# Performance work log

Hardware: AMD Instinct MI355X
Metric: run time of the kernel (lower is better)

The kernel has to match this reference:

```python
import jax, jax.numpy as jnp
import numpy as np

N_NODES = 100000
N_GRAPHS = 64
NEG_SLOPE = 0.1


def lrelu(x):
    return jnp.where(x > 0, x, NEG_SLOPE * x)


def gcn_layer(x, W, b, src, dst, deg_inv_sqrt):
    # PyG GCNConv: x' = D^-1/2 (A + I) D^-1/2 (x W) + b
    h = x @ W  # [N, out]
    norm = (deg_inv_sqrt[src] * deg_inv_sqrt[dst])[:, None]  # [E, 1]
    agg = jax.ops.segment_sum(h[src] * norm, dst, num_segments=N_NODES)
    agg = agg + h * (deg_inv_sqrt ** 2)[:, None]  # self-loop contribution
    return agg + b


def setup_inputs() -> dict:
    key = jax.random.key(0)
    ks = jax.random.split(key, 12)
    E = 1600000
    x = jax.random.normal(ks[0], (N_NODES, 128), dtype=jnp.float32)
    edge_index = jax.random.randint(ks[1], (2, E), 0, N_NODES, dtype=jnp.int32)
    batch = jnp.sort(jax.random.randint(ks[2], (N_NODES,), 0, N_GRAPHS, dtype=jnp.int32))

    def glorot(k, shape):
        fan_in, fan_out = shape
        s = jnp.sqrt(6.0 / (fan_in + fan_out))
        return jax.random.uniform(k, shape, jnp.float32, -s, s)

    return {
        "x": x,
        "edge_index": edge_index,
        "batch": batch,
        "W1": glorot(ks[3], (128, 32)),
        "b1": jnp.zeros((32,), jnp.float32),
        "W2": glorot(ks[4], (32, 64)),
        "b2": jnp.zeros((64,), jnp.float32),
        "Wl1": glorot(ks[5], (64, 128)),
        "bl1": jnp.zeros((128,), jnp.float32),
        "Wl2": glorot(ks[6], (128, 64)),
        "bl2": jnp.zeros((64,), jnp.float32),
        "Wl3": glorot(ks[7], (64, 1)),
        "bl3": jnp.zeros((1,), jnp.float32),
    }


def reference(x, edge_index, batch, W1, b1, W2, b2, Wl1, bl1, Wl2, bl2, Wl3, bl3):
    src, dst = edge_index[0], edge_index[1]
    # degree with self-loops (symmetric norm, all edge weights = 1)
    deg = jax.ops.segment_sum(jnp.ones_like(src, dtype=x.dtype), dst, num_segments=N_NODES) + 1.0
    deg_inv_sqrt = jax.lax.rsqrt(deg)

    h = lrelu(gcn_layer(x, W1, b1, src, dst, deg_inv_sqrt))
    h = gcn_layer(h, W2, b2, src, dst, deg_inv_sqrt)
    g = jax.ops.segment_max(h, batch, num_segments=N_GRAPHS)  # global max pool [G, 64]
    g = lrelu(g @ Wl1 + bl1)
    g = lrelu(g @ Wl2 + bl2)
    return g @ Wl3 + bl3  # [G, 1]
```

## Files before the change

### kernel.cpp

```cpp
#include <hip/hip_runtime.h>
#include <hip/hip_fp16.h>
#include <math.h>

#define N_NODES 100000
#define N_EDGES 1600000
#define N_GRAPHS 64
#define NB 391
#define CAP 5504

__device__ __forceinline__ unsigned f2o(float f) {
    unsigned u = __float_as_uint(f);
    return (u & 0x80000000u) ? ~u : (u | 0x80000000u);
}
__device__ __forceinline__ float o2f(unsigned u) {
    return (u & 0x80000000u) ? __uint_as_float(u & 0x7fffffffu) : __uint_as_float(~u);
}

__device__ __forceinline__ float4 cvt8(float2 raw) {
    __half2 h0 = ((const __half2*)&raw)[0];
    __half2 h1 = ((const __half2*)&raw)[1];
    float2 f0 = __half22float2(h0);
    float2 f1 = __half22float2(h1);
    return make_float4(f0.x, f0.y, f1.x, f1.y);
}
__device__ __forceinline__ float4 loadh8(const __half* p) {
    return cvt8(*(const float2*)p);
}
__device__ __forceinline__ void storeh8(__half* p, float4 v) {
    __half2 o0 = __floats2half2_rn(v.x, v.y);
    __half2 o1 = __floats2half2_rn(v.z, v.w);
    float2 ow;
    ((__half2*)&ow)[0] = o0;
    ((__half2*)&ow)[1] = o1;
    *(float2*)p = ow;
}

typedef _Float16 h2r __attribute__((ext_vector_type(2)));
typedef _Float16 h4  __attribute__((ext_vector_type(4)));
union HB { float4 f4; h2r h[4]; };
union H4 { float2 f2; h4 h; };

__global__ __launch_bounds__(256) void bucket_kernel(const int* __restrict__ src, const int* __restrict__ dst,
                                                     int* __restrict__ bucketCursor, unsigned* __restrict__ ebuf) {
    __shared__ int hist[NB];
    __shared__ int cur[NB];
    int tid = threadIdx.x;
    for (int b = tid; b < NB; b += 256) hist[b] = 0;
    __syncthreads();
    int e0 = blockIdx.x * 3200;
    for (int i = tid; i < 3200; i += 256) {
        int d = dst[e0 + i];
        atomicAdd(&hist[d >> 8], 1);
    }
    __syncthreads();
    for (int b = tid; b < NB; b += 256) {
        int h = hist[b];
        cur[b] = h ? atomicAdd(&bucketCursor[b], h) : 0;
    }
    __syncthreads();
    for (int i = tid; i < 3200; i += 256) {
        int d = dst[e0 + i];
        int s = src[e0 + i];
        int bu = d >> 8;
        int pos = atomicAdd(&cur[bu], 1);
        if (pos < CAP)
            ebuf[(size_t)bu * CAP + pos] = ((unsigned)(d & 255) << 24) | (unsigned)s;
    }
}

__global__ __launch_bounds__(256) void csr_kernel(const unsigned* __restrict__ ebuf,
                                                  const int* __restrict__ bucketCursor,
                                                  int* __restrict__ colb, int* __restrict__ rowptr,
                                                  int* __restrict__ cnt, float* __restrict__ dis) {
    __shared__ unsigned stage[CAP];
    __shared__ int c256[256], row256[256], cur256[256];
    int b = blockIdx.x;
    int tid = threadIdx.x;
    int M = bucketCursor[b];
    if (M > CAP) M = CAP;
    c256[tid] = 0;
    __syncthreads();
    const unsigned* eb = ebuf + (size_t)b * CAP;
    for (int i = tid; i < M; i += 256) atomicAdd(&c256[eb[i] >> 24], 1);
    __syncthreads();
    if (tid < 64) {
        int c0 = c256[tid * 4], c1 = c256[tid * 4 + 1], c2 = c256[tid * 4 + 2], c3 = c256[tid * 4 + 3];
        int s = c0 + c1 + c2 + c3;
        int inc = s;
        #pragma unroll
        for (int o = 1; o < 64; o <<= 1) {
            int v = __shfl_up(inc, o, 64);
            if (tid >= o) inc += v;
        }
        int ex = inc - s;
        row256[tid * 4] = ex;
        row256[tid * 4 + 1] = ex + c0;
        row256[tid * 4 + 2] = ex + c0 + c1;
        row256[tid * 4 + 3] = ex + c0 + c1 + c2;
    }
    __syncthreads();
    cur256[tid] = row256[tid];
    int node = (b << 8) + tid;
    if (node < N_NODES) {
        int c = c256[tid];
        cnt[node] = c;
        dis[node] = rsqrtf((float)(c + 1));
        rowptr[node] = b * CAP + row256[tid];
    }
    __syncthreads();
    for (int i = tid; i < M; i += 256) {
        unsigned p = eb[i];
        int slot = atomicAdd(&cur256[p >> 24], 1);
        stage[slot] = p & 0xFFFFFFu;
    }
    __syncthreads();
    for (int i = tid; i < M; i += 256) colb[b * CAP + i] = (int)stage[i];
}

__global__ __launch_bounds__(256) void gemm1_kernel(const float* __restrict__ x, const float* __restrict__ W1,
                                                    const float* __restrict__ dis, __half* __restrict__ hs1h) {
    __shared__ __half xsh[128][136];
    __shared__ __half wth[32][136];
    int tid = threadIdx.x;
    int r0 = blockIdx.x * 128;
    for (int idx = tid; idx < 128 * 32; idx += 256) {
        int k = idx >> 5, j = idx & 31;
        wth[j][k] = __float2half_rn(W1[idx]);
    }
    for (int idx = tid; idx < 128 * 32; idx += 256) {
        int r = idx >> 5, c4 = idx & 31;
        int gr = r0 + r;
        float4 v = (gr < N_NODES) ? ((const float4*)x)[(size_t)gr * 32 + c4] : make_float4(0.f, 0.f, 0.f, 0.f);
        __half* p = &xsh[r][c4 * 4];
        *(__half2*)p       = __floats2half2_rn(v.x, v.y);
        *(__half2*)(p + 2) = __floats2half2_rn(v.z, v.w);
    }
    __syncthreads();
    int jg = tid & 7;
    int rg = tid >> 3;
    float acc[4][4];
    #pragma unroll
    for (int i = 0; i < 4; i++)
        #pragma unroll
        for (int j = 0; j < 4; j++) acc[i][j] = 0.f;
    for (int kc = 0; kc < 128; kc += 8) {
        HB xr[4], wr[4];
        #pragma unroll
        for (int ri = 0; ri < 4; ri++) xr[ri].f4 = *(const float4*)&xsh[rg + 32 * ri][kc];
        #pragma unroll
        for (int jj = 0; jj < 4; jj++) wr[jj].f4 = *(const float4*)&wth[jg * 4 + jj][kc];
        #pragma unroll
        for (int ri = 0; ri < 4; ri++) {
            #pragma unroll
            for (int jj = 0; jj < 4; jj++) {
                #pragma unroll
                for (int t = 0; t < 4; t++) {
#if defined(__has_builtin) && __has_builtin(__builtin_amdgcn_fdot2)
                    acc[ri][jj] = __builtin_amdgcn_fdot2(xr[ri].h[t], wr[jj].h[t], acc[ri][jj], false);
#else
                    acc[ri][jj] += (float)xr[ri].h[t][0] * (float)wr[jj].h[t][0]
                                 + (float)xr[ri].h[t][1] * (float)wr[jj].h[t][1];
#endif
                }
            }
        }
    }
    #pragma unroll
    for (int ri = 0; ri < 4; ri++) {
        int gr = r0 + rg + 32 * ri;
        if (gr < N_NODES) {
            float dr = dis[gr];
            float2 ow;
            ((__half2*)&ow)[0] = __floats2half2_rn(dr * acc[ri][0], dr * acc[ri][1]);
            ((__half2*)&ow)[1] = __floats2half2_rn(dr * acc[ri][2], dr * acc[ri][3]);
            *(float2*)&hs1h[(size_t)gr * 32 + jg * 4] = ow;
        }
    }
}

__global__ __launch_bounds__(256) void agg1_kernel(const __half* __restrict__ hs1h, const int* __restrict__ colb,
                                                   const int* __restrict__ rowptr, const int* __restrict__ cnt,
                                                   const float* __restrict__ dis, const float* __restrict__ b1,
                                                   __half* __restrict__ t1h) {
    int tid = threadIdx.x;
    int wid = tid >> 6;
    int lane = tid & 63;
    int half = lane >> 5;
    int es = (lane >> 3) & 3;
    int q = lane & 7;
    int w = blockIdx.x * 4 + wid;
    int r0 = w * 4;

    H4 z; z.f2 = make_float2(0.f, 0.f);
    int r = r0 + half;
    int st = rowptr[r];
    int n = cnt[r];
    H4 pS = z, p0 = z, p1 = z, p2 = z, p3 = z, p4 = z, p5 = z;
    if (es == 0) pS.f2 = *(const float2*)(hs1h + (size_t)r * 32 + q * 4);
    {
        int e0 = es, e1 = 4 + es, e2 = 8 + es, e3 = 12 + es, e4 = 16 + es, e5 = 20 + es;
        if (e0 < n) p0.f2 = *(const float2*)(hs1h + (size_t)colb[st + e0] * 32 + q * 4);
        if (e1 < n) p1.f2 = *(const float2*)(hs1h + (size_t)colb[st + e1] * 32 + q * 4);
        if (e2 < n) p2.f2 = *(const float2*)(hs1h + (size_t)colb[st + e2] * 32 + q * 4);
        if (e3 < n) p3.f2 = *(const float2*)(hs1h + (size_t)colb[st + e3] * 32 + q * 4);
        if (e4 < n) p4.f2 = *(const float2*)(hs1h + (size_t)colb[st + e4] * 32 + q * 4);
        if (e5 < n) p5.f2 = *(const float2*)(hs1h + (size_t)colb[st + e5] * 32 + q * 4);
    }
    #pragma unroll
    for (int i = 0; i < 2; i++) {
        int rA = r;
        int stA = st, nA = n;
        H4 rS = pS, v0 = p0, v1 = p1, v2 = p2, v3 = p3, v4 = p4, v5 = p5;
        pS = z; p0 = z; p1 = z; p2 = z; p3 = z; p4 = z; p5 = z;
        if (i == 0) {
            r = r0 + 2 + half;
            st = rowptr[r];
            n = cnt[r];
            if (es == 0) pS.f2 = *(const float2*)(hs1h + (size_t)r * 32 + q * 4);
            int e0 = es, e1 = 4 + es, e2 = 8 + es, e3 = 12 + es, e4 = 16 + es, e5 = 20 + es;
            if (e0 < n) p0.f2 = *(const float2*)(hs1h + (size_t)colb[st + e0] * 32 + q * 4);
            if (e1 < n) p1.f2 = *(const float2*)(hs1h + (size_t)colb[st + e1] * 32 + q * 4);
            if (e2 < n) p2.f2 = *(const float2*)(hs1h + (size_t)colb[st + e2] * 32 + q * 4);
            if (e3 < n) p3.f2 = *(const float2*)(hs1h + (size_t)colb[st + e3] * 32 + q * 4);
            if (e4 < n) p4.f2 = *(const float2*)(hs1h + (size_t)colb[st + e4] * 32 + q * 4);
            if (e5 < n) p5.f2 = *(const float2*)(hs1h + (size_t)colb[st + e5] * 32 + q * 4);
        }
        h4 sh = (rS.h + (v0.h + v1.h)) + ((v2.h + v3.h) + (v4.h + v5.h));
        float4 a = make_float4((float)sh.x, (float)sh.y, (float)sh.z, (float)sh.w);
        for (int k = 24; k < nA; k += 8) {
            int e0 = k + es, e1 = k + 4 + es;
            if (e0 < nA) {
                float4 v = loadh8(hs1h + (size_t)colb[stA + e0] * 32 + q * 4);
                a.x += v.x; a.y += v.y; a.z += v.z; a.w += v.w;
            }
            if (e1 < nA) {
                float4 v = loadh8(hs1h + (size_t)colb[stA + e1] * 32 + q * 4);
                a.x += v.x; a.y += v.y; a.z += v.z; a.w += v.w;
            }
        }
        #pragma unroll
        for (int m = 8; m <= 16; m <<= 1) {
            a.x += __shfl_xor(a.x, m, 64);
            a.y += __shfl_xor(a.y, m, 64);
            a.z += __shfl_xor(a.z, m, 64);
            a.w += __shfl_xor(a.w, m, 64);
        }
        if (es == 0) {
            float4 bv = *(const float4*)&b1[q * 4];
            float dr = dis[rA];
            float4 v;
            v.x = dr * a.x + bv.x; v.y = dr * a.y + bv.y; v.z = dr * a.z + bv.z; v.w = dr * a.w + bv.w;
            v.x = v.x > 0.f ? v.x : 0.1f * v.x;
            v.y = v.y > 0.f ? v.y : 0.1f * v.y;
            v.z = v.z > 0.f ? v.z : 0.1f * v.z;
            v.w = v.w > 0.f ? v.w : 0.1f * v.w;
            v.x *= dr; v.y *= dr; v.z *= dr; v.w *= dr;
            storeh8(t1h + (size_t)rA * 32 + q * 4, v);
        }
    }
}

__global__ __launch_bounds__(256) void agg2_kernel(const __half* __restrict__ t1h, const int* __restrict__ colb,
                                                   const int* __restrict__ rowptr, const int* __restrict__ cnt,
                                                   const float* __restrict__ dis,
                                                   float* __restrict__ agg32) {
    int tid = threadIdx.x;
    int wid = tid >> 6;
    int lane = tid & 63;
    int half = lane >> 5;
    int es = (lane >> 3) & 3;
    int q = lane & 7;
    int w = blockIdx.x * 4 + wid;
    int r0 = w * 4;

    H4 z; z.f2 = make_float2(0.f, 0.f);
    int r = r0 + half;
    int st = rowptr[r];
    int n = cnt[r];
    H4 pS = z, p0 = z, p1 = z, p2 = z, p3 = z, p4 = z, p5 = z;
    if (es == 0) pS.f2 = *(const float2*)(t1h + (size_t)r * 32 + q * 4);
    {
        int e0 = es, e1 = 4 + es, e2 = 8 + es, e3 = 12 + es, e4 = 16 + es, e5 = 20 + es;
        if (e0 < n) p0.f2 = *(const float2*)(t1h + (size_t)colb[st + e0] * 32 + q * 4);
        if (e1 < n) p1.f2 = *(const float2*)(t1h + (size_t)colb[st + e1] * 32 + q * 4);
        if (e2 < n) p2.f2 = *(const float2*)(t1h + (size_t)colb[st + e2] * 32 + q * 4);
        if (e3 < n) p3.f2 = *(const float2*)(t1h + (size_t)colb[st + e3] * 32 + q * 4);
        if (e4 < n) p4.f2 = *(const float2*)(t1h + (size_t)colb[st + e4] * 32 + q * 4);
        if (e5 < n) p5.f2 = *(const float2*)(t1h + (size_t)colb[st + e5] * 32 + q * 4);
    }
    #pragma unroll
    for (int i = 0; i < 2; i++) {
        int rA = r;
        int stA = st, nA = n;
        H4 rS = pS, v0 = p0, v1 = p1, v2 = p2, v3 = p3, v4 = p4, v5 = p5;
        pS = z; p0 = z; p1 = z; p2 = z; p3 = z; p4 = z; p5 = z;
        if (i == 0) {
            r = r0 + 2 + half;
            st = rowptr[r];
            n = cnt[r];
            if (es == 0) pS.f2 = *(const float2*)(t1h + (size_t)r * 32 + q * 4);
            int e0 = es, e1 = 4 + es, e2 = 8 + es, e3 = 12 + es, e4 = 16 + es, e5 = 20 + es;
            if (e0 < n) p0.f2 = *(const float2*)(t1h + (size_t)colb[st + e0] * 32 + q * 4);
            if (e1 < n) p1.f2 = *(const float2*)(t1h + (size_t)colb[st + e1] * 32 + q * 4);
            if (e2 < n) p2.f2 = *(const float2*)(t1h + (size_t)colb[st + e2] * 32 + q * 4);
            if (e3 < n) p3.f2 = *(const float2*)(t1h + (size_t)colb[st + e3] * 32 + q * 4);
            if (e4 < n) p4.f2 = *(const float2*)(t1h + (size_t)colb[st + e4] * 32 + q * 4);
            if (e5 < n) p5.f2 = *(const float2*)(t1h + (size_t)colb[st + e5] * 32 + q * 4);
        }
        h4 sh = (rS.h + (v0.h + v1.h)) + ((v2.h + v3.h) + (v4.h + v5.h));
        float4 a = make_float4((float)sh.x, (float)sh.y, (float)sh.z, (float)sh.w);
        for (int k = 24; k < nA; k += 8) {
            int e0 = k + es, e1 = k + 4 + es;
            if (e0 < nA) {
                float4 v = loadh8(t1h + (size_t)colb[stA + e0] * 32 + q * 4);
                a.x += v.x; a.y += v.y; a.z += v.z; a.w += v.w;
            }
            if (e1 < nA) {
                float4 v = loadh8(t1h + (size_t)colb[stA + e1] * 32 + q * 4);
                a.x += v.x; a.y += v.y; a.z += v.z; a.w += v.w;
            }
        }
        #pragma unroll
        for (int m = 8; m <= 16; m <<= 1) {
            a.x += __shfl_xor(a.x, m, 64);
            a.y += __shfl_xor(a.y, m, 64);
            a.z += __shfl_xor(a.z, m, 64);
            a.w += __shfl_xor(a.w, m, 64);
        }
        if (es == 0) {
            float dr = dis[rA];
            float4 o = make_float4(dr * a.x, dr * a.y, dr * a.z, dr * a.w);
            *(float4*)&agg32[(size_t)rA * 32 + q * 4] = o;
        }
    }
}

__global__ __launch_bounds__(256) void gemm2p_kernel(const float* __restrict__ agg32, const float* __restrict__ W2,
                                                     const float* __restrict__ b2, const int* __restrict__ batch,
                                                     unsigned* __restrict__ gbufu) {
    __shared__ float as1[64][32];
    __shared__ float w2s[32][64];
    __shared__ float red[4][64];
    int tid = threadIdx.x;
    int r0 = blockIdx.x * 64;
    for (int idx = tid; idx < 32 * 64; idx += 256) w2s[idx >> 6][idx & 63] = W2[idx];
    for (int idx = tid; idx < 64 * 8; idx += 256) {
        int rl = idx >> 3, qc = idx & 7;
        int gr = r0 + rl;
        float4 v = (gr < N_NODES) ? ((const float4*)agg32)[(size_t)gr * 8 + qc] : make_float4(0.f, 0.f, 0.f, 0.f);
        *(float4*)&as1[rl][qc * 4] = v;
    }
    __syncthreads();
    int j = tid & 63;
    int rq = tid >> 6;
    float w2c[32];
    #pragma unroll
    for (int k = 0; k < 32; k++) w2c[k] = w2s[k][j];
    float bj = b2[j];
    int rend = (r0 + 64 <= N_NODES) ? 64 : (N_NODES - r0);
    int gfirst = batch[r0];
    int glast = batch[r0 + rend - 1];
    bool uni = (gfirst == glast);
    float runmax = -INFINITY;
    for (int i = 0; i < 16; i++) {
        int rl = rq + i * 4;
        if (rl >= rend) break;
        float acc = bj;
        #pragma unroll
        for (int kc = 0; kc < 32; kc += 4) {
            float4 av = *(const float4*)&as1[rl][kc];
            acc += av.x * w2c[kc] + av.y * w2c[kc + 1] + av.z * w2c[kc + 2] + av.w * w2c[kc + 3];
        }
        if (uni) runmax = fmaxf(runmax, acc);
        else atomicMax(&gbufu[batch[r0 + rl] * 64 + j], f2o(acc));
    }
    if (uni) {
        red[rq][j] = runmax;
        __syncthreads();
        if (tid < 64) {
            float m = fmaxf(fmaxf(red[0][tid], red[1][tid]), fmaxf(red[2][tid], red[3][tid]));
            atomicMax(&gbufu[gfirst * 64 + tid], f2o(m));
        }
    }
}

__global__ __launch_bounds__(256) void mlp_kernel(const unsigned* __restrict__ gbufu,
                                                  const float* __restrict__ Wl1, const float* __restrict__ bl1,
                                                  const float* __restrict__ Wl2, const float* __restrict__ bl2,
                                                  const float* __restrict__ Wl3, const float* __restrict__ bl3,
                                                  float* __restrict__ out) {
    __shared__ float A[64][64];
    __shared__ float B[64][128];
    int tid = threadIdx.x;
    for (int idx = tid; idx < 64 * 64; idx += 256) A[idx >> 6][idx & 63] = o2f(gbufu[idx]);
    __syncthreads();
    {
        int j = tid & 127;
        int rg = tid >> 7;
        float wc[64];
        #pragma unroll
        for (int k = 0; k < 64; k++) wc[k] = Wl1[k * 128 + j];
        float bj = bl1[j];
        for (int r = rg; r < 64; r += 2) {
            float acc = bj;
            #pragma unroll
            for (int kc = 0; kc < 64; kc += 4) {
                float4 av = *(const float4*)&A[r][kc];
                acc += av.x * wc[kc] + av.y * wc[kc + 1] + av.z * wc[kc + 2] + av.w * wc[kc + 3];
            }
            B[r][j] = acc > 0.f ? acc : 0.1f * acc;
        }
    }
    __syncthreads();
    {
        int j = tid & 63;
        int rg = tid >> 6;
        float wc[128];
        #pragma unroll
        for (int k = 0; k < 128; k++) wc[k] = Wl2[k * 64 + j];
        float bj = bl2[j];
        for (int r = rg; r < 64; r += 4) {
            float acc = bj;
            #pragma unroll
            for (int kc = 0; kc < 128; kc += 4) {
                float4 bv = *(const float4*)&B[r][kc];
                acc += bv.x * wc[kc] + bv.y * wc[kc + 1] + bv.z * wc[kc + 2] + bv.w * wc[kc + 3];
            }
            A[r][j] = acc > 0.f ? acc : 0.1f * acc;
        }
    }
    __syncthreads();
    if (tid < 64) {
        int r = tid;
        float acc = bl3[0];
        #pragma unroll
        for (int k = 0; k < 64; k++) acc += A[r][k] * Wl3[k];
        out[r] = acc;
    }
}

extern "C" void kernel_launch(void* const* d_in, const int* in_sizes, int n_in,
                              void* d_out, int out_size, void* d_ws, size_t ws_size,
                              hipStream_t stream) {
    (void)in_sizes; (void)n_in; (void)out_size; (void)ws_size;
    const float* x    = (const float*)d_in[0];
    const int*   edge = (const int*)d_in[1];
    const int*   batch= (const int*)d_in[2];
    const float* W1   = (const float*)d_in[3];
    const float* b1   = (const float*)d_in[4];
    const float* W2   = (const float*)d_in[5];
    const float* b2   = (const float*)d_in[6];
    const float* Wl1  = (const float*)d_in[7];
    const float* bl1  = (const float*)d_in[8];
    const float* Wl2  = (const float*)d_in[9];
    const float* bl2  = (const float*)d_in[10];
    const float* Wl3  = (const float*)d_in[11];
    const float* bl3  = (const float*)d_in[12];
    const int* srcp = edge;
    const int* dstp = edge + N_EDGES;

    char* ws = (char*)d_ws;
    int*      bucketCursor = (int*)ws;
    unsigned* gbufu        = (unsigned*)(bucketCursor + NB);
    size_t zeroed = (size_t)(NB + N_GRAPHS * 64) * 4;
    size_t off = (zeroed + 255) & ~(size_t)255;
    auto alloc = [&](size_t bytes) { char* p = ws + off; off = (off + bytes + 255) & ~(size_t)255; return p; };
    float*    dis    = (float*)alloc((size_t)N_NODES * 4);
    int*      cnt    = (int*)alloc((size_t)N_NODES * 4);
    int*      rowptr = (int*)alloc((size_t)N_NODES * 4);
    unsigned* ebuf   = (unsigned*)alloc((size_t)NB * CAP * 4);
    int*      colb   = (int*)alloc((size_t)NB * CAP * 4);
    __half*   hs1h   = (__half*)alloc((size_t)N_NODES * 32 * 2);
    __half*   t1h    = (__half*)alloc((size_t)N_NODES * 32 * 2);
    float*    agg32  = (float*)alloc((size_t)N_NODES * 32 * 4);

    hipMemsetAsync(ws, 0, zeroed, stream);

    bucket_kernel<<<500, 256, 0, stream>>>(srcp, dstp, bucketCursor, ebuf);
    csr_kernel   <<<NB, 256, 0, stream>>>(ebuf, bucketCursor, colb, rowptr, cnt, dis);
    gemm1_kernel <<<(N_NODES + 127) / 128, 256, 0, stream>>>(x, W1, dis, hs1h);
    agg1_kernel  <<<6250, 256, 0, stream>>>(hs1h, colb, rowptr, cnt, dis, b1, t1h);
    agg2_kernel  <<<6250, 256, 0, stream>>>(t1h, colb, rowptr, cnt, dis, agg32);
    gemm2p_kernel<<<(N_NODES + 63) / 64, 256, 0, stream>>>(agg32, W2, b2, batch, gbufu);
    mlp_kernel   <<<1, 256, 0, stream>>>(gbufu, Wl1, bl1, Wl2, bl2, Wl3, bl3, (float*)d_out);
}
```

Measured before the change: 279.7 us.

## Split 32-wide half features into two 16-column halves aggregated in separate passes

The layer-1 GEMM output and the hidden activations are stored as two separate 16-column fp16 arrays. Each aggregation kernel now runs twice, once per half, with 8 edges per step and 4 lanes per row. The smaller per-node row (32 bytes) is meant to halve the gathered working set per pass so it fits better in cache and makes random gathers cheaper. In exchange the CSR indices are read twice and there are two extra kernel launches. The remainder-edge accumulation also moves from fp32 to fp16 packed adds, which may lose precision on high-degree nodes.

```diff
diff --git a/kernel.cpp b/kernel.cpp
--- a/kernel.cpp
+++ b/kernel.cpp
@@ -16,16 +16,6 @@
     return (u & 0x80000000u) ? __uint_as_float(u & 0x7fffffffu) : __uint_as_float(~u);
 }
 
-__device__ __forceinline__ float4 cvt8(float2 raw) {
-    __half2 h0 = ((const __half2*)&raw)[0];
-    __half2 h1 = ((const __half2*)&raw)[1];
-    float2 f0 = __half22float2(h0);
-    float2 f1 = __half22float2(h1);
-    return make_float4(f0.x, f0.y, f1.x, f1.y);
-}
-__device__ __forceinline__ float4 loadh8(const __half* p) {
-    return cvt8(*(const float2*)p);
-}
 __device__ __forceinline__ void storeh8(__half* p, float4 v) {
     __half2 o0 = __floats2half2_rn(v.x, v.y);
     __half2 o1 = __floats2half2_rn(v.z, v.w);
@@ -118,7 +108,8 @@
 }
 
 __global__ __launch_bounds__(256) void gemm1_kernel(const float* __restrict__ x, const float* __restrict__ W1,
-                                                    const float* __restrict__ dis, __half* __restrict__ hs1h) {
+                                                    const float* __restrict__ dis,
+                                                    __half* __restrict__ hs1a, __half* __restrict__ hs1b) {
     __shared__ __half xsh[128][136];
     __shared__ __half wth[32][136];
     int tid = threadIdx.x;
@@ -165,6 +156,8 @@
             }
         }
     }
+    __half* hb = (jg < 4) ? hs1a : hs1b;
+    int qc = (jg & 3) * 4;
     #pragma unroll
     for (int ri = 0; ri < 4; ri++) {
         int gr = r0 + rg + 32 * ri;
@@ -173,21 +166,21 @@
             float2 ow;
             ((__half2*)&ow)[0] = __floats2half2_rn(dr * acc[ri][0], dr * acc[ri][1]);
             ((__half2*)&ow)[1] = __floats2half2_rn(dr * acc[ri][2], dr * acc[ri][3]);
-            *(float2*)&hs1h[(size_t)gr * 32 + jg * 4] = ow;
-        }
-    }
-}
-
-__global__ __launch_bounds__(256) void agg1_kernel(const __half* __restrict__ hs1h, const int* __restrict__ colb,
-                                                   const int* __restrict__ rowptr, const int* __restrict__ cnt,
-                                                   const float* __restrict__ dis, const float* __restrict__ b1,
-                                                   __half* __restrict__ t1h) {
+            *(float2*)&hb[(size_t)gr * 16 + qc] = ow;
+        }
+    }
+}
+
+__global__ __launch_bounds__(256) void aggL1_kernel(const __half* __restrict__ in, const int* __restrict__ colb,
+                                                    const int* __restrict__ rowptr, const int* __restrict__ cnt,
+                                                    const float* __restrict__ dis, const float* __restrict__ b1p,
+                                                    __half* __restrict__ out) {
     int tid = threadIdx.x;
     int wid = tid >> 6;
     int lane = tid & 63;
     int half = lane >> 5;
-    int es = (lane >> 3) & 3;
-    int q = lane & 7;
+    int es = (lane >> 2) & 7;
+    int q = lane & 3;
     int w = blockIdx.x * 4 + wid;
     int r0 = w * 4;
 
@@ -195,49 +188,40 @@
     int r = r0 + half;
     int st = rowptr[r];
     int n = cnt[r];
-    H4 pS = z, p0 = z, p1 = z, p2 = z, p3 = z, p4 = z, p5 = z;
-    if (es == 0) pS.f2 = *(const float2*)(hs1h + (size_t)r * 32 + q * 4);
+    H4 pS = z, p0 = z, p1 = z, p2 = z;
+    if (es == 0) pS.f2 = *(const float2*)(in + (size_t)r * 16 + q * 4);
     {
-        int e0 = es, e1 = 4 + es, e2 = 8 + es, e3 = 12 + es, e4 = 16 + es, e5 = 20 + es;
-        if (e0 < n) p0.f2 = *(const float2*)(hs1h + (size_t)colb[st + e0] * 32 + q * 4);
-        if (e1 < n) p1.f2 = *(const float2*)(hs1h + (size_t)colb[st + e1] * 32 + q * 4);
-        if (e2 < n) p2.f2 = *(const float2*)(hs1h + (size_t)colb[st + e2] * 32 + q * 4);
-        if (e3 < n) p3.f2 = *(const float2*)(hs1h + (size_t)colb[st + e3] * 32 + q * 4);
-        if (e4 < n) p4.f2 = *(const float2*)(hs1h + (size_t)colb[st + e4] * 32 + q * 4);
-        if (e5 < n) p5.f2 = *(const float2*)(hs1h + (size_t)colb[st + e5] * 32 + q * 4);
+        int e0 = es, e1 = 8 + es, e2 = 16 + es;
+        if (e0 < n) p0.f2 = *(const float2*)(in + (size_t)colb[st + e0] * 16 + q * 4);
+        if (e1 < n) p1.f2 = *(const float2*)(in + (size_t)colb[st + e1] * 16 + q * 4);
+        if (e2 < n) p2.f2 = *(const float2*)(in + (size_t)colb[st + e2] * 16 + q * 4);
     }
     #pragma unroll
     for (int i = 0; i < 2; i++) {
         int rA = r;
         int stA = st, nA = n;
-        H4 rS = pS, v0 = p0, v1 = p1, v2 = p2, v3 = p3, v4 = p4, v5 = p5;
-        pS = z; p0 = z; p1 = z; p2 = z; p3 = z; p4 = z; p5 = z;
+        H4 rS = pS, v0 = p0, v1 = p1, v2 = p2;
+        pS = z; p0 = z; p1 = z; p2 = z;
         if (i == 0) {
             r = r0 + 2 + half;
             st = rowptr[r];
             n = cnt[r];
-            if (es == 0) pS.f2 = *(const float2*)(hs1h + (size_t)r * 32 + q * 4);
-            int e0 = es, e1 = 4 + es, e2 = 8 + es, e3 = 12 + es, e4 = 16 + es, e5 = 20 + es;
-            if (e0 < n) p0.f2 = *(const float2*)(hs1h + (size_t)colb[st + e0] * 32 + q * 4);
-            if (e1 < n) p1.f2 = *(const float2*)(hs1h + (size_t)colb[st + e1] * 32 + q * 4);
-            if (e2 < n) p2.f2 = *(const float2*)(hs1h + (size_t)colb[st + e2] * 32 + q * 4);
-            if (e3 < n) p3.f2 = *(const float2*)(hs1h + (size_t)colb[st + e3] * 32 + q * 4);
-            if (e4 < n) p4.f2 = *(const float2*)(hs1h + (size_t)colb[st + e4] * 32 + q * 4);
-            if (e5 < n) p5.f2 = *(const float2*)(hs1h + (size_t)colb[st + e5] * 32 + q * 4);
-        }
-        h4 sh = (rS.h + (v0.h + v1.h)) + ((v2.h + v3.h) + (v4.h + v5.h));
-        float4 a = make_float4((float)sh.x, (float)sh.y, (float)sh.z, (float)sh.w);
+            if (es == 0) pS.f2 = *(const float2*)(in + (size_t)r * 16 + q * 4);
+            int e0 = es, e1 = 8 + es, e2 = 16 + es;
+            if (e0 < n) p0.f2 = *(const float2*)(in + (size_t)colb[st + e0] * 16 + q * 4);
+            if (e1 < n) p1.f2 = *(const float2*)(in + (size_t)colb[st + e1] * 16 + q * 4);
+            if (e2 < n) p2.f2 = *(const float2*)(in + (size_t)colb[st + e2] * 16 + q * 4);
+        }
+        H4 u; u.h = (rS.h + v0.h) + (v1.h + v2.h);
         for (int k = 24; k < nA; k += 8) {
-            int e0 = k + es, e1 = k + 4 + es;
-            if (e0 < nA) {
-                float4 v = loadh8(hs1h + (size_t)colb[stA + e0] * 32 + q * 4);
-                a.x += v.x; a.y += v.y; a.z += v.z; a.w += v.w;
-            }
-            if (e1 < nA) {
-                float4 v = loadh8(hs1h + (size_t)colb[stA + e1] * 32 + q * 4);
-                a.x += v.x; a.y += v.y; a.z += v.z; a.w += v.w;
-            }
-        }
+            int e0 = k + es;
+            if (e0 < nA) { H4 t; t.f2 = *(const float2*)(in + (size_t)colb[stA + e0] * 16 + q * 4); u.h = u.h + t.h; }
+        }
+        H4 o;
+        o.f2.x = __shfl_xor(u.f2.x, 4, 64);
+        o.f2.y = __shfl_xor(u.f2.y, 4, 64);
+        u.h = u.h + o.h;
+        float4 a = make_float4((float)u.h.x, (float)u.h.y, (float)u.h.z, (float)u.h.w);
         #pragma unroll
         for (int m = 8; m <= 16; m <<= 1) {
             a.x += __shfl_xor(a.x, m, 64);
@@ -246,7 +230,7 @@
             a.w += __shfl_xor(a.w, m, 64);
         }
         if (es == 0) {
-            float4 bv = *(const float4*)&b1[q * 4];
+            float4 bv = *(const float4*)&b1p[q * 4];
             float dr = dis[rA];
             float4 v;
             v.x = dr * a.x + bv.x; v.y = dr * a.y + bv.y; v.z = dr * a.z + bv.z; v.w = dr * a.w + bv.w;
@@ -255,21 +239,21 @@
             v.z = v.z > 0.f ? v.z : 0.1f * v.z;
             v.w = v.w > 0.f ? v.w : 0.1f * v.w;
             v.x *= dr; v.y *= dr; v.z *= dr; v.w *= dr;
-            storeh8(t1h + (size_t)rA * 32 + q * 4, v);
-        }
-    }
-}
-
-__global__ __launch_bounds__(256) void agg2_kernel(const __half* __restrict__ t1h, const int* __restrict__ colb,
-                                                   const int* __restrict__ rowptr, const int* __restrict__ cnt,
-                                                   const float* __restrict__ dis,
-                                                   float* __restrict__ agg32) {
+            storeh8(out + (size_t)rA * 16 + q * 4, v);
+        }
+    }
+}
+
+__global__ __launch_bounds__(256) void aggL2_kernel(const __half* __restrict__ in, const int* __restrict__ colb,
+                                                    const int* __restrict__ rowptr, const int* __restrict__ cnt,
+                                                    const float* __restrict__ dis,
+                                                    float* __restrict__ out) {
     int tid = threadIdx.x;
     int wid = tid >> 6;
     int lane = tid & 63;
     int half = lane >> 5;
-    int es = (lane >> 3) & 3;
-    int q = lane & 7;
+    int es = (lane >> 2) & 7;
+    int q = lane & 3;
     int w = blockIdx.x * 4 + wid;
     int r0 = w * 4;
 
@@ -277,49 +261,40 @@
     int r = r0 + half;
     int st = rowptr[r];
     int n = cnt[r];
-    H4 pS = z, p0 = z, p1 = z, p2 = z, p3 = z, p4 = z, p5 = z;
-    if (es == 0) pS.f2 = *(const float2*)(t1h + (size_t)r * 32 + q * 4);
+    H4 pS = z, p0 = z, p1 = z, p2 = z;
+    if (es == 0) pS.f2 = *(const float2*)(in + (size_t)r * 16 + q * 4);
     {
-        int e0 = es, e1 = 4 + es, e2 = 8 + es, e3 = 12 + es, e4 = 16 + es, e5 = 20 + es;
-        if (e0 < n) p0.f2 = *(const float2*)(t1h + (size_t)colb[st + e0] * 32 + q * 4);
-        if (e1 < n) p1.f2 = *(const float2*)(t1h + (size_t)colb[st + e1] * 32 + q * 4);
-        if (e2 < n) p2.f2 = *(const float2*)(t1h + (size_t)colb[st + e2] * 32 + q * 4);
-        if (e3 < n) p3.f2 = *(const float2*)(t1h + (size_t)colb[st + e3] * 32 + q * 4);
-        if (e4 < n) p4.f2 = *(const float2*)(t1h + (size_t)colb[st + e4] * 32 + q * 4);
-        if (e5 < n) p5.f2 = *(const float2*)(t1h + (size_t)colb[st + e5] * 32 + q * 4);
+        int e0 = es, e1 = 8 + es, e2 = 16 + es;
+        if (e0 < n) p0.f2 = *(const float2*)(in + (size_t)colb[st + e0] * 16 + q * 4);
+        if (e1 < n) p1.f2 = *(const float2*)(in + (size_t)colb[st + e1] * 16 + q * 4);
+        if (e2 < n) p2.f2 = *(const float2*)(in + (size_t)colb[st + e2] * 16 + q * 4);
     }
     #pragma unroll
     for (int i = 0; i < 2; i++) {
         int rA = r;
         int stA = st, nA = n;
-        H4 rS = pS, v0 = p0, v1 = p1, v2 = p2, v3 = p3, v4 = p4, v5 = p5;
-        pS = z; p0 = z; p1 = z; p2 = z; p3 = z; p4 = z; p5 = z;
+        H4 rS = pS, v0 = p0, v1 = p1, v2 = p2;
+        pS = z; p0 = z; p1 = z; p2 = z;
         if (i == 0) {
             r = r0 + 2 + half;
             st = rowptr[r];
             n = cnt[r];
-            if (es == 0) pS.f2 = *(const float2*)(t1h + (size_t)r * 32 + q * 4);
-            int e0 = es, e1 = 4 + es, e2 = 8 + es, e3 = 12 + es, e4 = 16 + es, e5 = 20 + es;
-            if (e0 < n) p0.f2 = *(const float2*)(t1h + (size_t)colb[st + e0] * 32 + q * 4);
-            if (e1 < n) p1.f2 = *(const float2*)(t1h + (size_t)colb[st + e1] * 32 + q * 4);
-            if (e2 < n) p2.f2 = *(const float2*)(t1h + (size_t)colb[st + e2] * 32 + q * 4);
-            if (e3 < n) p3.f2 = *(const float2*)(t1h + (size_t)colb[st + e3] * 32 + q * 4);
-            if (e4 < n) p4.f2 = *(const float2*)(t1h + (size_t)colb[st + e4] * 32 + q * 4);
-            if (e5 < n) p5.f2 = *(const float2*)(t1h + (size_t)colb[st + e5] * 32 + q * 4);
-        }
-        h4 sh = (rS.h + (v0.h + v1.h)) + ((v2.h + v3.h) + (v4.h + v5.h));
-        float4 a = make_float4((float)sh.x, (float)sh.y, (float)sh.z, (float)sh.w);
+            if (es == 0) pS.f2 = *(const float2*)(in + (size_t)r * 16 + q * 4);
+            int e0 = es, e1 = 8 + es, e2 = 16 + es;
+            if (e0 < n) p0.f2 = *(const float2*)(in + (size_t)colb[st + e0] * 16 + q * 4);
+            if (e1 < n) p1.f2 = *(const float2*)(in + (size_t)colb[st + e1] * 16 + q * 4);
+            if (e2 < n) p2.f2 = *(const float2*)(in + (size_t)colb[st + e2] * 16 + q * 4);
+        }
+        H4 u; u.h = (rS.h + v0.h) + (v1.h + v2.h);
         for (int k = 24; k < nA; k += 8) {
-            int e0 = k + es, e1 = k + 4 + es;
-            if (e0 < nA) {
-                float4 v = loadh8(t1h + (size_t)colb[stA + e0] * 32 + q * 4);
-                a.x += v.x; a.y += v.y; a.z += v.z; a.w += v.w;
-            }
-            if (e1 < nA) {
-                float4 v = loadh8(t1h + (size_t)colb[stA + e1] * 32 + q * 4);
-                a.x += v.x; a.y += v.y; a.z += v.z; a.w += v.w;
-            }
-        }
+            int e0 = k + es;
+            if (e0 < nA) { H4 t; t.f2 = *(const float2*)(in + (size_t)colb[stA + e0] * 16 + q * 4); u.h = u.h + t.h; }
+        }
+        H4 o;
+        o.f2.x = __shfl_xor(u.f2.x, 4, 64);
+        o.f2.y = __shfl_xor(u.f2.y, 4, 64);
+        u.h = u.h + o.h;
+        float4 a = make_float4((float)u.h.x, (float)u.h.y, (float)u.h.z, (float)u.h.w);
         #pragma unroll
         for (int m = 8; m <= 16; m <<= 1) {
             a.x += __shfl_xor(a.x, m, 64);
@@ -329,8 +304,8 @@
         }
         if (es == 0) {
             float dr = dis[rA];
-            float4 o = make_float4(dr * a.x, dr * a.y, dr * a.z, dr * a.w);
-            *(float4*)&agg32[(size_t)rA * 32 + q * 4] = o;
+            float4 ov = make_float4(dr * a.x, dr * a.y, dr * a.z, dr * a.w);
+            *(float4*)&out[(size_t)rA * 32 + q * 4] = ov;
         }
     }
 }
@@ -470,17 +445,21 @@
     int*      rowptr = (int*)alloc((size_t)N_NODES * 4);
     unsigned* ebuf   = (unsigned*)alloc((size_t)NB * CAP * 4);
     int*      colb   = (int*)alloc((size_t)NB * CAP * 4);
-    __half*   hs1h   = (__half*)alloc((size_t)N_NODES * 32 * 2);
-    __half*   t1h    = (__half*)alloc((size_t)N_NODES * 32 * 2);
+    __half*   hs1a   = (__half*)alloc((size_t)N_NODES * 16 * 2);
+    __half*   hs1b   = (__half*)alloc((size_t)N_NODES * 16 * 2);
+    __half*   t1a    = (__half*)alloc((size_t)N_NODES * 16 * 2);
+    __half*   t1b    = (__half*)alloc((size_t)N_NODES * 16 * 2);
     float*    agg32  = (float*)alloc((size_t)N_NODES * 32 * 4);
 
     hipMemsetAsync(ws, 0, zeroed, stream);
 
     bucket_kernel<<<500, 256, 0, stream>>>(srcp, dstp, bucketCursor, ebuf);
     csr_kernel   <<<NB, 256, 0, stream>>>(ebuf, bucketCursor, colb, rowptr, cnt, dis);
-    gemm1_kernel <<<(N_NODES + 127) / 128, 256, 0, stream>>>(x, W1, dis, hs1h);
-    agg1_kernel  <<<6250, 256, 0, stream>>>(hs1h, colb, rowptr, cnt, dis, b1, t1h);
-    agg2_kernel  <<<6250, 256, 0, stream>>>(t1h, colb, rowptr, cnt, dis, agg32);
+    gemm1_kernel <<<(N_NODES + 127) / 128, 256, 0, stream>>>(x, W1, dis, hs1a, hs1b);
+    aggL1_kernel <<<6250, 256, 0, stream>>>(hs1a, colb, rowptr, cnt, dis, b1,      t1a);
+    aggL1_kernel <<<6250, 256, 0, stream>>>(hs1b, colb, rowptr, cnt, dis, b1 + 16, t1b);
+    aggL2_kernel <<<6250, 256, 0, stream>>>(t1a, colb, rowptr, cnt, dis, agg32);
+    aggL2_kernel <<<6250, 256, 0, stream>>>(t1b, colb, rowptr, cnt, dis, agg32 + 16);
     gemm2p_kernel<<<(N_NODES + 63) / 64, 256, 0, stream>>>(agg32, W2, b2, batch, gbufu);
     mlp_kernel   <<<1, 256, 0, stream>>>(gbufu, Wl1, bl1, Wl2, bl2, Wl3, bl3, (float*)d_out);
 }
```

Result: slower. 291.7 us (+4.3%).
